# Optimization experiments

Measured on AMD Instinct MI355X. Metric: run time of the kernel, lower is better.

Reference implementation:

```python
import jax, jax.numpy as jnp
import numpy as np

N_HEAD = 16
ROPE_BASE = 10000.0

def rotate_half(x):
    half = x.shape[-1] // 2
    return jnp.concatenate((-x[..., half:], x[..., :half]), axis=-1)

def rope_freqs(T, head_dim, dtype):
    inv_freq = 1.0 / (ROPE_BASE ** (jnp.arange(0, head_dim, 2, dtype=jnp.float32) / head_dim))
    t = jnp.arange(T, dtype=jnp.float32)
    freqs = t[:, None] * inv_freq[None, :]          # [T, head_dim//2]
    emb = jnp.concatenate((freqs, freqs), axis=-1)  # [T, head_dim]
    return emb.astype(dtype)

def setup_inputs() -> dict:
    key = jax.random.key(0)
    ks = jax.random.split(key, 9)
    B, T, C = 2, 2048, 1024
    s = 1.0 / np.sqrt(C)
    return {
        'x':  jax.random.normal(ks[0], (B, T, C), jnp.float32),
        'Wq': jax.random.normal(ks[1], (C, C), jnp.float32) * s,
        'bq': jnp.zeros((C,), jnp.float32),
        'Wk': jax.random.normal(ks[2], (C, C), jnp.float32) * s,
        'bk': jnp.zeros((C,), jnp.float32),
        'Wv': jax.random.normal(ks[3], (C, C), jnp.float32) * s,
        'bv': jnp.zeros((C,), jnp.float32),
        'Wp': jax.random.normal(ks[4], (C, C), jnp.float32) * s,
        'bp': jnp.zeros((C,), jnp.float32),
    }

def reference(x, Wq, bq, Wk, bk, Wv, bv, Wp, bp):
    B, T, C = x.shape
    H = N_HEAD
    D = C // H
    # torch Linear: y = x @ W.T + b
    def heads(y):
        return y.reshape(B, T, H, D).transpose(0, 2, 1, 3)  # [B,H,T,D]
    q = heads(x @ Wq.T + bq)
    k = heads(x @ Wk.T + bk)
    v = heads(x @ Wv.T + bv)
    # inline RoPE
    emb = rope_freqs(T, D, x.dtype)          # [T, D]
    cos, sin = jnp.cos(emb), jnp.sin(emb)
    q = q * cos + rotate_half(q) * sin
    k = k * cos + rotate_half(k) * sin
    # full T x T scores with causal masked softmax
    att = jnp.einsum('bhtd,bhsd->bhts', q, k) * (1.0 / jnp.sqrt(jnp.array(D, x.dtype)))
    causal = jnp.tril(jnp.ones((T, T), bool))
    att = jnp.where(causal[None, None], att, jnp.array(-jnp.inf, att.dtype))
    att = jax.nn.softmax(att, axis=-1)
    y = jnp.einsum('bhts,bhsd->bhtd', att, v)  # [B,H,T,D]
    y = y.transpose(0, 2, 1, 3).reshape(B, T, C)
    return y @ Wp.T + bp
```

## Files before the change

kernel.cpp:

```cpp
#include <hip/hip_runtime.h>
#include <hip/hip_bf16.h>
#include <stdint.h>

typedef unsigned short u16;
typedef __attribute__((ext_vector_type(8))) short bf16x8;
typedef __attribute__((ext_vector_type(4))) float f32x4;

typedef const __attribute__((address_space(1))) unsigned int* gu32p;
typedef __attribute__((address_space(3))) unsigned int* lu32p;

__device__ __forceinline__ void gl_lds16(const u16* g, u16* l) {
  __builtin_amdgcn_global_load_lds((gu32p)(const void*)g, (lu32p)(void*)l, 16, 0, 0);
}

__device__ __forceinline__ u16 f2bf(float f) {
  union { float f; unsigned u; } v; v.f = f;
  unsigned r = v.u + 0x7fffu + ((v.u >> 16) & 1u);
  return (u16)(r >> 16);
}
__device__ __forceinline__ void st2bf(u16* p0, u16* p1, float a, float b) {
  union { __hip_bfloat162 h; u16 u[2]; } cv;
  cv.h = __float22bfloat162_rn(make_float2(a, b));
  *p0 = cv.u[0]; *p1 = cv.u[1];
}

__global__ void convert_kernel(const float4* __restrict__ x, const float4* __restrict__ wq,
                               const float4* __restrict__ wk, const float4* __restrict__ wv,
                               const float4* __restrict__ wp,
                               u16* __restrict__ xb, u16* __restrict__ wqb, u16* __restrict__ wkb,
                               u16* __restrict__ wvb, u16* __restrict__ wpb,
                               float2* __restrict__ tab) {
  int i = blockIdx.x * 256 + threadIdx.x;
  const int NX = 1048576, NW = 262144, NCONV = NX + 4 * NW;
  if (i >= NCONV) {
    int j = i - NCONV;
    int d = j & 31, t = j >> 5;
    float ang = (float)t * expf(-0.28782313662425572f * (float)d);
    tab[j] = make_float2(cosf(ang), sinf(ang));
    return;
  }
  const float4* src; u16* dst; int off;
  if (i < NX)            { src = x;  dst = xb;  off = i; }
  else if (i < NX + NW)  { src = wq; dst = wqb; off = i - NX; }
  else if (i < NX + 2*NW){ src = wk; dst = wkb; off = i - NX - NW; }
  else if (i < NX + 3*NW){ src = wv; dst = wvb; off = i - NX - 2*NW; }
  else                   { src = wp; dst = wpb; off = i - NX - 3*NW; }
  float4 v = src[off];
  ushort4 ov = make_ushort4(f2bf(v.x), f2bf(v.y), f2bf(v.z), f2bf(v.w));
  *(ushort4*)&dst[off * 4] = ov;
}

template<int FUSE_ROPE, int OUT_BF16, int TRANS_V>
__global__ __launch_bounds__(256) void gemm_bt_kernel(
    const u16* __restrict__ A,
    const u16* __restrict__ B0, const u16* __restrict__ B1, const u16* __restrict__ B2,
    const float* __restrict__ bias0, const float* __restrict__ bias1, const float* __restrict__ bias2,
    void* out0, void* out1, void* out2, const float2* __restrict__ tab)
{
  __shared__ __align__(16) u16 As[4096];
  __shared__ __align__(16) u16 Bs[4096];
  const int z = blockIdx.z;
  const u16* Bw = (z == 0) ? B0 : (z == 1) ? B1 : B2;
  const float* bias = (z == 0) ? bias0 : (z == 1) ? bias1 : bias2;
  void* outv = (z == 0) ? out0 : (z == 1) ? out1 : out2;
  const int tid = threadIdx.x, lane = tid & 63, w = tid >> 6;
  const int wr = w >> 1, wc = w & 1;
  const int quad = lane >> 4, l15 = lane & 15;
  const int m0 = blockIdx.y * 128, n0 = blockIdx.x * 128;
  const int sr = lane >> 2, sc = (lane & 3) * 8;

  f32x4 acc[4][4] = {};
  for (int k0 = 0; k0 < 1024; k0 += 32) {
    __syncthreads();
    #pragma unroll
    for (int p = 0; p < 2; p++) {
      gl_lds16(A  + (m0 + p*64 + w*16 + sr) * 1024 + k0 + sc, As + p*2048 + w*512);
      gl_lds16(Bw + (n0 + p*64 + w*16 + sr) * 1024 + k0 + sc, Bs + p*2048 + w*512);
    }
    __syncthreads();
    bf16x8 af[4], bfr[4];
    #pragma unroll
    for (int mt = 0; mt < 4; mt++)
      af[mt] = *(const bf16x8*)&As[(wr*64 + mt*16 + l15) * 32 + quad*8];
    #pragma unroll
    for (int nt = 0; nt < 4; nt++)
      bfr[nt] = *(const bf16x8*)&Bs[(wc*64 + nt*16 + l15) * 32 + quad*8];
    #pragma unroll
    for (int mt = 0; mt < 4; mt++)
      #pragma unroll
      for (int nt = 0; nt < 4; nt++)
        acc[mt][nt] = __builtin_amdgcn_mfma_f32_16x16x32_bf16(af[mt], bfr[nt], acc[mt][nt], 0, 0, 0);
  }

  if (TRANS_V && z == 2) {
    const int bb = m0 >> 11, tg0 = (m0 & 2047) + wr*64 + quad*4;
    #pragma unroll
    for (int nt = 0; nt < 4; nt++) {
      const int c = n0 + wc*64 + nt*16 + l15;
      const float bv = bias[c];
      u16* vrow = (u16*)outv + (size_t)(bb*1024 + c) * 2048 + tg0;
      #pragma unroll
      for (int mt = 0; mt < 4; mt++) {
        ushort4 pk;
        pk.x = f2bf(acc[mt][nt][0] + bv); pk.y = f2bf(acc[mt][nt][1] + bv);
        pk.z = f2bf(acc[mt][nt][2] + bv); pk.w = f2bf(acc[mt][nt][3] + bv);
        *(ushort4*)&vrow[mt*16] = pk;
      }
    }
    return;
  }

  #pragma unroll
  for (int mt = 0; mt < 4; mt++) {
    #pragma unroll
    for (int r = 0; r < 4; r++) {
      const int row = m0 + wr*64 + mt*16 + quad*4 + r;
      float v[4];
      #pragma unroll
      for (int nt = 0; nt < 4; nt++)
        v[nt] = acc[mt][nt][r] + bias[n0 + wc*64 + nt*16 + l15];
      if (FUSE_ROPE && z < 2) {
        const int t = row & 2047;
        #pragma unroll
        for (int nt = 0; nt < 2; nt++) {
          const int d = nt*16 + l15;
          float2 cs = tab[t*32 + d];
          float x0 = v[nt], x1 = v[nt+2];
          v[nt]   = x0 * cs.x - x1 * cs.y;
          v[nt+2] = x1 * cs.x + x0 * cs.y;
        }
      }
      #pragma unroll
      for (int nt = 0; nt < 4; nt++) {
        const int col = n0 + wc*64 + nt*16 + l15;
        if (OUT_BF16) ((u16*)outv)[row * 1024 + col] = f2bf(v[nt]);
        else          ((float*)outv)[row * 1024 + col] = v[nt];
      }
    }
  }
}

__global__ __launch_bounds__(512) void attn_kernel(
    const u16* __restrict__ qg, const u16* __restrict__ kg,
    const u16* __restrict__ vtg, u16* __restrict__ yg)
{
  __shared__ __align__(16) u16 K_lds[2][128 * 64];
  __shared__ __align__(16) u16 V_lds[2][64 * 128];
  __shared__ __align__(16) u16 P_lds[8][16 * 128];
  const int x = blockIdx.x;
  const int hh = blockIdx.y, b = blockIdx.z;
  const int tid = threadIdx.x, lane = tid & 63, w = tid >> 6;
  const int wt = w >> 2;
  const int quad = lane >> 4, l15 = lane & 15;
  const int bh = b * (2048 * 1024) + hh * 64;
  const int vtb = (b * 16 + hh) * 131072;

  const int qtA = x, qtB = 15 - x;
  const int qt_w = wt ? qtB : qtA;
  const int wl = w & 3;

  bf16x8 qf[2][2];
  #pragma unroll
  for (int rg = 0; rg < 2; rg++) {
    const int qrow = qt_w*128 + rg*64 + wl*16 + l15;
    qf[rg][0] = *(const bf16x8*)&qg[bh + qrow*1024 + quad*8];
    qf[rg][1] = *(const bf16x8*)&qg[bh + qrow*1024 + 32 + quad*8];
  }
  f32x4 o[2][4] = {};
  f32x4 l5[2] = {};

  bf16x8 ones;
  #pragma unroll
  for (int i2 = 0; i2 < 8; i2++) ones[i2] = (short)0x3F80;

  auto stage = [&](int j, int bf) {
    {
      const int r = w*16 + (lane >> 3) + ((lane >> 2) & 1) * 8;
    }
  };

  const float c = 0.18033688011112042f;

  auto do_stage = [&](int j, int bf) {
    #pragma unroll
    for (int p = 0; p < 2; p++) {
      const int seg = w*2 + p;
      const int r = seg*8 + (lane >> 3);
      const int g = (lane & 7) ^ (r & 7);
      gl_lds16(kg + bh + (j*128 + r) * 1024 + g*8, &K_lds[bf][seg*512]);
    }
    #pragma unroll
    for (int p = 0; p < 2; p++) {
      const int seg = w*2 + p;
      const int r = seg*4 + (lane >> 4);
      const int g = (lane & 15) ^ (r & 15);
      gl_lds16(vtg + vtb + r * 2048 + j*128 + g*8, &V_lds[bf][seg*512]);
    }
  };

  do_stage(0, 0);
  for (int j = 0; j <= qtB; j++) {
    __syncthreads();
    if (j < qtB) do_stage(j + 1, (j + 1) & 1);
    const int bf = j & 1;
    if (wt == 0 && j > qtA) continue;
    const bool diag = (j == qt_w);

    #pragma unroll
    for (int rg = 0; rg < 2; rg++) {
      f32x4 s[8];
      #pragma unroll
      for (int nt = 0; nt < 8; nt++) {
        const int krow = (nt*16 + l15) * 64;
        const int g0 = ((quad)     ^ (l15 & 7)) * 8;
        const int g1 = ((4 + quad) ^ (l15 & 7)) * 8;
        bf16x8 kf0 = *(const bf16x8*)&K_lds[bf][krow + g0];
        bf16x8 kf1 = *(const bf16x8*)&K_lds[bf][krow + g1];
        f32x4 z = {};
        z = __builtin_amdgcn_mfma_f32_16x16x32_bf16(qf[rg][0], kf0, z, 0, 0, 0);
        z = __builtin_amdgcn_mfma_f32_16x16x32_bf16(qf[rg][1], kf1, z, 0, 0, 0);
        s[nt] = z;
      }
      if (diag) {
        const int trow = rg*64 + wl*16 + quad*4;
        #pragma unroll
        for (int nt = 0; nt < 8; nt++)
          #pragma unroll
          for (int r = 0; r < 4; r++)
            if (nt*16 + l15 > trow + r) s[nt][r] = -1e30f;
      }
      #pragma unroll
      for (int r = 0; r < 4; r++) {
        const int R = quad*4 + r;
        u16* pp = &P_lds[w][R*128 + (l15 & 7)];
        #pragma unroll
        for (int nt = 0; nt < 8; nt += 2) {
          float p0 = exp2f(s[nt][r] * c);
          float p1 = exp2f(s[nt+1][r] * c);
          const int g0 = ((nt*2     + (l15 >> 3)) ^ (R & 7)) * 8;
          const int g1 = (((nt+1)*2 + (l15 >> 3)) ^ (R & 7)) * 8;
          st2bf(pp + g0, pp + g1, p0, p1);
        }
      }
      #pragma unroll
      for (int ss = 0; ss < 4; ss++) {
        const int pg = ((ss*4 + quad) ^ (l15 & 7)) * 8;
        bf16x8 pf = *(const bf16x8*)&P_lds[w][l15*128 + pg];
        l5[rg] = __builtin_amdgcn_mfma_f32_16x16x32_bf16(pf, ones, l5[rg], 0, 0, 0);
        #pragma unroll
        for (int dt = 0; dt < 4; dt++) {
          const int vg = ((ss*4 + quad) ^ l15) * 8;
          bf16x8 vf = *(const bf16x8*)&V_lds[bf][(dt*16 + l15)*128 + vg];
          o[rg][dt] = __builtin_amdgcn_mfma_f32_16x16x32_bf16(pf, vf, o[rg][dt], 0, 0, 0);
        }
      }
    }
  }

  #pragma unroll
  for (int rg = 0; rg < 2; rg++)
    #pragma unroll
    for (int r = 0; r < 4; r++) {
      float inv = 1.0f / l5[rg][r];
      u16* yr = &yg[bh + (qt_w*128 + rg*64 + wl*16 + quad*4 + r) * 1024 + l15];
      st2bf(yr,      yr + 16, o[rg][0][r] * inv, o[rg][1][r] * inv);
      st2bf(yr + 32, yr + 48, o[rg][2][r] * inv, o[rg][3][r] * inv);
    }
}

extern "C" void kernel_launch(void* const* d_in, const int* in_sizes, int n_in,
                              void* d_out, int out_size, void* d_ws, size_t ws_size,
                              hipStream_t stream) {
  const float* x  = (const float*)d_in[0];
  const float* Wq = (const float*)d_in[1];
  const float* bq = (const float*)d_in[2];
  const float* Wk = (const float*)d_in[3];
  const float* bk = (const float*)d_in[4];
  const float* Wv = (const float*)d_in[5];
  const float* bv = (const float*)d_in[6];
  const float* Wp = (const float*)d_in[7];
  const float* bp = (const float*)d_in[8];

  char* ws = (char*)d_ws;
  u16* xb  = (u16*)(ws);
  u16* wqb = (u16*)(ws + (8u  << 20));
  u16* wkb = (u16*)(ws + (10u << 20));
  u16* wvb = (u16*)(ws + (12u << 20));
  u16* wpb = (u16*)(ws + (14u << 20));
  u16* qb  = (u16*)(ws + (16u << 20));
  u16* kb  = (u16*)(ws + (24u << 20));
  u16* vtb = (u16*)(ws + (32u << 20));
  float2* tab = (float2*)(ws + (40u << 20));
  u16* yb = xb;

  convert_kernel<<<8448, 256, 0, stream>>>((const float4*)x, (const float4*)Wq, (const float4*)Wk,
                                           (const float4*)Wv, (const float4*)Wp,
                                           xb, wqb, wkb, wvb, wpb, tab);
  gemm_bt_kernel<1, 1, 1><<<dim3(8, 32, 3), 256, 0, stream>>>(xb, wqb, wkb, wvb, bq, bk, bv,
                                                              (void*)qb, (void*)kb, (void*)vtb, tab);
  attn_kernel<<<dim3(8, 16, 2), 512, 0, stream>>>(qb, kb, vtb, yb);
  gemm_bt_kernel<0, 0, 0><<<dim3(8, 32, 1), 256, 0, stream>>>(yb, wpb, wpb, wpb, bp, bp, bp,
                                                              (void*)d_out, (void*)d_out, (void*)d_out, tab);
}
```

Baseline: 226.3 us.

## Double-buffer GEMM LDS tiles and share K/V fragments across attention row groups

```diff
diff --git a/kernel.cpp b/kernel.cpp
--- a/kernel.cpp
+++ b/kernel.cpp
@@ -57,8 +57,8 @@
     const float* __restrict__ bias0, const float* __restrict__ bias1, const float* __restrict__ bias2,
     void* out0, void* out1, void* out2, const float2* __restrict__ tab)
 {
-  __shared__ __align__(16) u16 As[4096];
-  __shared__ __align__(16) u16 Bs[4096];
+  __shared__ __align__(16) u16 As[2][4096];
+  __shared__ __align__(16) u16 Bs[2][4096];
   const int z = blockIdx.z;
   const u16* Bw = (z == 0) ? B0 : (z == 1) ? B1 : B2;
   const float* bias = (z == 0) ? bias0 : (z == 1) ? bias1 : bias2;
@@ -69,22 +69,28 @@
   const int m0 = blockIdx.y * 128, n0 = blockIdx.x * 128;
   const int sr = lane >> 2, sc = (lane & 3) * 8;
 
+  auto stg = [&](int kt, int bf) {
+    const int k0 = kt * 32;
+    #pragma unroll
+    for (int p = 0; p < 2; p++) {
+      gl_lds16(A  + (m0 + p*64 + w*16 + sr) * 1024 + k0 + sc, &As[bf][p*2048 + w*512]);
+      gl_lds16(Bw + (n0 + p*64 + w*16 + sr) * 1024 + k0 + sc, &Bs[bf][p*2048 + w*512]);
+    }
+  };
+
   f32x4 acc[4][4] = {};
-  for (int k0 = 0; k0 < 1024; k0 += 32) {
+  stg(0, 0);
+  for (int kt = 0; kt < 32; kt++) {
     __syncthreads();
-    #pragma unroll
-    for (int p = 0; p < 2; p++) {
-      gl_lds16(A  + (m0 + p*64 + w*16 + sr) * 1024 + k0 + sc, As + p*2048 + w*512);
-      gl_lds16(Bw + (n0 + p*64 + w*16 + sr) * 1024 + k0 + sc, Bs + p*2048 + w*512);
-    }
-    __syncthreads();
+    if (kt < 31) stg(kt + 1, (kt + 1) & 1);
+    const int bf = kt & 1;
     bf16x8 af[4], bfr[4];
     #pragma unroll
     for (int mt = 0; mt < 4; mt++)
-      af[mt] = *(const bf16x8*)&As[(wr*64 + mt*16 + l15) * 32 + quad*8];
+      af[mt] = *(const bf16x8*)&As[bf][(wr*64 + mt*16 + l15) * 32 + quad*8];
     #pragma unroll
     for (int nt = 0; nt < 4; nt++)
-      bfr[nt] = *(const bf16x8*)&Bs[(wc*64 + nt*16 + l15) * 32 + quad*8];
+      bfr[nt] = *(const bf16x8*)&Bs[bf][(wc*64 + nt*16 + l15) * 32 + quad*8];
     #pragma unroll
     for (int mt = 0; mt < 4; mt++)
       #pragma unroll
@@ -146,7 +152,7 @@
 {
   __shared__ __align__(16) u16 K_lds[2][128 * 64];
   __shared__ __align__(16) u16 V_lds[2][64 * 128];
-  __shared__ __align__(16) u16 P_lds[8][16 * 128];
+  __shared__ __align__(16) u16 P_lds[8][2][16 * 128];
   const int x = blockIdx.x;
   const int hh = blockIdx.y, b = blockIdx.z;
   const int tid = threadIdx.x, lane = tid & 63, w = tid >> 6;
@@ -173,12 +179,6 @@
   #pragma unroll
   for (int i2 = 0; i2 < 8; i2++) ones[i2] = (short)0x3F80;
 
-  auto stage = [&](int j, int bf) {
-    {
-      const int r = w*16 + (lane >> 3) + ((lane >> 2) & 1) * 8;
-    }
-  };
-
   const float c = 0.18033688011112042f;
 
   auto do_stage = [&](int j, int bf) {
@@ -206,53 +206,61 @@
     if (wt == 0 && j > qtA) continue;
     const bool diag = (j == qt_w);
 
-    #pragma unroll
-    for (int rg = 0; rg < 2; rg++) {
-      f32x4 s[8];
-      #pragma unroll
-      for (int nt = 0; nt < 8; nt++) {
-        const int krow = (nt*16 + l15) * 64;
-        const int g0 = ((quad)     ^ (l15 & 7)) * 8;
-        const int g1 = ((4 + quad) ^ (l15 & 7)) * 8;
-        bf16x8 kf0 = *(const bf16x8*)&K_lds[bf][krow + g0];
-        bf16x8 kf1 = *(const bf16x8*)&K_lds[bf][krow + g1];
+    f32x4 s[2][8];
+    #pragma unroll
+    for (int nt = 0; nt < 8; nt++) {
+      const int krow = (nt*16 + l15) * 64;
+      const int g0 = ((quad)     ^ (l15 & 7)) * 8;
+      const int g1 = ((4 + quad) ^ (l15 & 7)) * 8;
+      bf16x8 kf0 = *(const bf16x8*)&K_lds[bf][krow + g0];
+      bf16x8 kf1 = *(const bf16x8*)&K_lds[bf][krow + g1];
+      #pragma unroll
+      for (int rg = 0; rg < 2; rg++) {
         f32x4 z = {};
         z = __builtin_amdgcn_mfma_f32_16x16x32_bf16(qf[rg][0], kf0, z, 0, 0, 0);
         z = __builtin_amdgcn_mfma_f32_16x16x32_bf16(qf[rg][1], kf1, z, 0, 0, 0);
-        s[nt] = z;
-      }
-      if (diag) {
+        s[rg][nt] = z;
+      }
+    }
+    if (diag) {
+      #pragma unroll
+      for (int rg = 0; rg < 2; rg++) {
         const int trow = rg*64 + wl*16 + quad*4;
         #pragma unroll
         for (int nt = 0; nt < 8; nt++)
           #pragma unroll
           for (int r = 0; r < 4; r++)
-            if (nt*16 + l15 > trow + r) s[nt][r] = -1e30f;
-      }
+            if (nt*16 + l15 > trow + r) s[rg][nt][r] = -1e30f;
+      }
+    }
+    #pragma unroll
+    for (int rg = 0; rg < 2; rg++)
       #pragma unroll
       for (int r = 0; r < 4; r++) {
         const int R = quad*4 + r;
-        u16* pp = &P_lds[w][R*128 + (l15 & 7)];
+        u16* pp = &P_lds[w][rg][R*128 + (l15 & 7)];
         #pragma unroll
         for (int nt = 0; nt < 8; nt += 2) {
-          float p0 = exp2f(s[nt][r] * c);
-          float p1 = exp2f(s[nt+1][r] * c);
+          float p0 = exp2f(s[rg][nt][r] * c);
+          float p1 = exp2f(s[rg][nt+1][r] * c);
           const int g0 = ((nt*2     + (l15 >> 3)) ^ (R & 7)) * 8;
           const int g1 = (((nt+1)*2 + (l15 >> 3)) ^ (R & 7)) * 8;
           st2bf(pp + g0, pp + g1, p0, p1);
         }
       }
-      #pragma unroll
-      for (int ss = 0; ss < 4; ss++) {
-        const int pg = ((ss*4 + quad) ^ (l15 & 7)) * 8;
-        bf16x8 pf = *(const bf16x8*)&P_lds[w][l15*128 + pg];
-        l5[rg] = __builtin_amdgcn_mfma_f32_16x16x32_bf16(pf, ones, l5[rg], 0, 0, 0);
-        #pragma unroll
-        for (int dt = 0; dt < 4; dt++) {
-          const int vg = ((ss*4 + quad) ^ l15) * 8;
-          bf16x8 vf = *(const bf16x8*)&V_lds[bf][(dt*16 + l15)*128 + vg];
-          o[rg][dt] = __builtin_amdgcn_mfma_f32_16x16x32_bf16(pf, vf, o[rg][dt], 0, 0, 0);
-        }
+    #pragma unroll
+    for (int ss = 0; ss < 4; ss++) {
+      const int pg = ((ss*4 + quad) ^ (l15 & 7)) * 8;
+      bf16x8 pf0 = *(const bf16x8*)&P_lds[w][0][l15*128 + pg];
+      bf16x8 pf1 = *(const bf16x8*)&P_lds[w][1][l15*128 + pg];
+      l5[0] = __builtin_amdgcn_mfma_f32_16x16x32_bf16(pf0, ones, l5[0], 0, 0, 0);
+      l5[1] = __builtin_amdgcn_mfma_f32_16x16x32_bf16(pf1, ones, l5[1], 0, 0, 0);
+      #pragma unroll
+      for (int dt = 0; dt < 4; dt++) {
+        const int vg = ((ss*4 + quad) ^ l15) * 8;
+        bf16x8 vf = *(const bf16x8*)&V_lds[bf][(dt*16 + l15)*128 + vg];
+        o[0][dt] = __builtin_amdgcn_mfma_f32_16x16x32_bf16(pf0, vf, o[0][dt], 0, 0, 0);
+        o[1][dt] = __builtin_amdgcn_mfma_f32_16x16x32_bf16(pf1, vf, o[1][dt], 0, 0, 0);
       }
     }
   }
```

Result: faster. 209.7 us (-7.3%).
